# Kernel tuning notes

Measured on AMD Instinct MI355X. Metric: run time of the kernel, lower is better.

Reference implementation:

```python
import jax, jax.numpy as jnp
import numpy as np

T, B, IN, H1, HB = 512, 256, 64, 128, 32  # seq, batch, input, LSTM width, bottleneck


def _lstm(x, w_ih, w_hh, b_ih, b_hh):
    """Single-layer unidirectional LSTM, time-major x: [T,B,in] -> [T,B,H].
    PyTorch gate order: i, f, g, o. Zero initial state."""
    H = w_hh.shape[1]
    # hoist input projection out of the scan: [T,B,4H]
    xg = jnp.einsum('tbi,gi->tbg', x, w_ih) + b_ih + b_hh

    def step(carry, xt):
        h, c = carry
        g = xt + h @ w_hh.T
        i, f, gg, o = jnp.split(g, 4, axis=-1)
        c = jax.nn.sigmoid(f) * c + jax.nn.sigmoid(i) * jnp.tanh(gg)
        h = jax.nn.sigmoid(o) * jnp.tanh(c)
        return (h, c), h

    h0 = jnp.zeros((x.shape[1], H), x.dtype)
    (_, _), hs = jax.lax.scan(step, (h0, h0), xg)
    return hs


def setup_inputs() -> dict:
    key = jax.random.key(0)
    ks = jax.random.split(key, 17)
    s = 0.05

    def p(k, shape):
        return jax.random.normal(k, shape, dtype=jnp.float32) * s

    return {
        'X': jax.random.normal(ks[0], (T, B, IN), dtype=jnp.float32),
        # en1: IN -> H1
        'w1_ih': p(ks[1], (4 * H1, IN)), 'w1_hh': p(ks[2], (4 * H1, H1)),
        'b1_ih': p(ks[3], (4 * H1,)), 'b1_hh': p(ks[4], (4 * H1,)),
        # en2: H1 -> HB
        'w2_ih': p(ks[5], (4 * HB, H1)), 'w2_hh': p(ks[6], (4 * HB, HB)),
        'b2_ih': p(ks[7], (4 * HB,)), 'b2_hh': p(ks[8], (4 * HB,)),
        # de1: HB -> H1
        'w3_ih': p(ks[9], (4 * H1, HB)), 'w3_hh': p(ks[10], (4 * H1, H1)),
        'b3_ih': p(ks[11], (4 * H1,)), 'b3_hh': p(ks[12], (4 * H1,)),
        # de2: H1 -> IN
        'w4_ih': p(ks[13], (4 * IN, H1)), 'w4_hh': p(ks[14], (4 * IN, IN)),
        'b4_ih': p(ks[15], (4 * IN,)), 'b4_hh': p(ks[16], (4 * IN,)),
    }


def reference(X, w1_ih, w1_hh, b1_ih, b1_hh, w2_ih, w2_hh, b2_ih, b2_hh,
              w3_ih, w3_hh, b3_ih, b3_hh, w4_ih, w4_hh, b4_ih, b4_hh):
    h = _lstm(X, w1_ih, w1_hh, b1_ih, b1_hh)      # [T,B,128]
    h = _lstm(h, w2_ih, w2_hh, b2_ih, b2_hh)      # [T,B,32]
    h = jnp.tanh(h)                               # bottleneck tanh
    h = _lstm(h, w3_ih, w3_hh, b3_ih, b3_hh)      # [T,B,128]
    out = _lstm(h, w4_ih, w4_hh, b4_ih, b4_hh)    # [T,B,64]
    return out
```

## Files before the change

kernel.cpp:

```cpp
#include <hip/hip_runtime.h>

#define T_STEPS 512
#define BATCH   256

typedef _Float16 f16;
typedef unsigned long long u64;
typedef __attribute__((ext_vector_type(8))) _Float16 f16x8;
typedef __attribute__((ext_vector_type(4))) _Float16 f16x4;
typedef __attribute__((ext_vector_type(4))) float    f32x4;

__device__ __forceinline__ float rcp_f(float x) { return __builtin_amdgcn_rcpf(x); }
__device__ __forceinline__ float sigmoid_f(float x) { return rcp_f(1.0f + __expf(-x)); }
__device__ __forceinline__ float tanh_f(float x) {
    return 1.0f - 2.0f * rcp_f(__expf(2.0f * x) + 1.0f);
}

__device__ __forceinline__ void barrier_lgkm() {
    asm volatile("s_waitcnt lgkmcnt(0)\n\ts_barrier" ::: "memory");
}
__device__ __forceinline__ void barrier_drain() {
    asm volatile("s_waitcnt vmcnt(0) lgkmcnt(0)\n\ts_barrier" ::: "memory");
}

__device__ __forceinline__ int  flag_load(const int* p) {
    return __hip_atomic_load(p, __ATOMIC_RELAXED, __HIP_MEMORY_SCOPE_AGENT);
}
__device__ __forceinline__ void flag_store(int* p, int v) {
    __hip_atomic_store(p, v, __ATOMIC_RELAXED, __HIP_MEMORY_SCOPE_AGENT);
}
__device__ __forceinline__ u64  panel_load(const u64* p) {
    return __hip_atomic_load(p, __ATOMIC_RELAXED, __HIP_MEMORY_SCOPE_AGENT);
}
__device__ __forceinline__ void panel_store(u64* p, u64 v) {
    __hip_atomic_store(p, v, __ATOMIC_RELAXED, __HIP_MEMORY_SCOPE_AGENT);
}

__device__ __forceinline__ u64 tanh4_f16(u64 v) {
    f16x4 h = __builtin_bit_cast(f16x4, v);
    f16x4 r;
#pragma unroll
    for (int i = 0; i < 4; ++i) r[i] = (f16)tanh_f((float)h[i]);
    return __builtin_bit_cast(u64, r);
}

template <int IN_DIM, int H, bool IN_F32, bool OUT_PANEL, bool IN_TANH>
__device__ __forceinline__ void lstm_layer_dev(
    char* sm,
    const void* __restrict__ xv,
    const int* in_flag,
    int* out_flag,
    const float* __restrict__ w_ih, const float* __restrict__ w_hh,
    const float* __restrict__ b_ih, const float* __restrict__ b_hh,
    void* __restrict__ outv,
    int group, int ltid)
{
    constexpr int KTX = IN_DIM / 32, KTH = H / 32, KT = KTX + KTH;
    constexpr int XP = IN_DIM + 8, HP = H + 8, NT = 4 * H;

    f16 (*xs)[16][XP] = (f16(*)[16][XP])sm;
    f16 (*hs)[16][HP] = (f16(*)[16][HP])(sm + 2 * 16 * XP * 2);

    const int wave = ltid >> 6, lane = ltid & 63;
    const int col = lane & 15, q = lane >> 4;
    const int bblk = group * 16;
    const int u = wave * 16 + col;

    f16x8 bw[4][KT];
#pragma unroll
    for (int g = 0; g < 4; ++g) {
        const int row = g * H + u;
#pragma unroll
        for (int kt = 0; kt < KTX; ++kt) {
            const float* p = w_ih + (size_t)row * IN_DIM + kt * 32 + q * 8;
            f16x8 v;
#pragma unroll
            for (int j = 0; j < 8; ++j) v[j] = (f16)p[j];
            bw[g][kt] = v;
        }
#pragma unroll
        for (int kt = 0; kt < KTH; ++kt) {
            const float* p = w_hh + (size_t)row * H + kt * 32 + q * 8;
            f16x8 v;
#pragma unroll
            for (int j = 0; j < 8; ++j) v[j] = (f16)p[j];
            bw[g][KTX + kt] = v;
        }
    }
    float bias[4];
#pragma unroll
    for (int g = 0; g < 4; ++g) bias[g] = b_ih[g * H + u] + b_hh[g * H + u];
    float cst[4] = {0.f, 0.f, 0.f, 0.f};

    constexpr int EPR = IN_DIM / 4;
    constexpr int NCH = 16 * EPR;
    constexpr int CPT = (NCH + NT - 1) / NT;
    constexpr long XADVB = (long)BATCH * IN_DIM * (IN_F32 ? 4 : 2);
    bool sv[CPT]; const char* sgp[CPT]; f16* slp[CPT];
    constexpr int LDSD = 16 * XP;
#pragma unroll
    for (int k = 0; k < CPT; ++k) {
        const int cc = ltid + k * NT;
        sv[k] = (cc < NCH);
        const int r_ = (cc < NCH ? cc : 0) / EPR;
        const int o_ = (cc < NCH ? cc : 0) % EPR;
        sgp[k] = (const char*)xv + ((size_t)(bblk + r_) * IN_DIM + o_ * 4) * (IN_F32 ? 4 : 2);
        slp[k] = &xs[0][r_][o_ * 4];
    }

    constexpr int OEPR = H / 4;
    u64* opg = nullptr;
    f16* olds = nullptr;
    float* outp_f32 = nullptr;
    if constexpr (OUT_PANEL) {
        const int orow = ltid / OEPR, ooff = ltid % OEPR;
        opg  = (u64*)((f16*)outv + (size_t)(bblk + orow) * H) + ooff;
        olds = &hs[0][orow][ooff * 4];
    } else {
        outp_f32 = (float*)outv + ((size_t)bblk + 4 * q) * H + u;
    }
    constexpr int HLDSD = 16 * HP;

    for (int i = ltid; i < 16 * HP; i += NT) hs[0][i / HP][i % HP] = (f16)0.f;
    int seen = 0;
    if constexpr (!IN_F32) {
        do { seen = flag_load(in_flag); } while (seen < 1);
    }
#pragma unroll
    for (int k = 0; k < CPT; ++k) {
        if (sv[k]) {
            if constexpr (IN_F32) {
                const f32x4 v = *reinterpret_cast<const f32x4*>(sgp[k]);
                f16x4 h4;
                h4[0] = (f16)v[0]; h4[1] = (f16)v[1]; h4[2] = (f16)v[2]; h4[3] = (f16)v[3];
                *reinterpret_cast<f16x4*>(slp[k]) = h4;
            } else {
                u64 v = panel_load((const u64*)sgp[k]);
                if constexpr (IN_TANH) v = tanh4_f16(v);
                *reinterpret_cast<u64*>(slp[k]) = v;
            }
            sgp[k] += XADVB;
        }
    }
    barrier_drain();

    float hold[4] = {0.f, 0.f, 0.f, 0.f};
    int pb = 0;
    for (int t = 0; t < T_STEPS; ++t) {
        if constexpr (OUT_PANEL) {
            if ((t & 3) == 0 && t >= 4 && ltid == 0) flag_store(out_flag, t - 1);
        }

        f32x4 xr32[CPT]; u64 xr16[CPT];
        const bool pf = (t + 1 < T_STEPS);
        if (pf) {
            if constexpr (!IN_F32) {
                if (seen < t + 2) {
                    do { seen = flag_load(in_flag); } while (seen < t + 2);
                }
            }
#pragma unroll
            for (int k = 0; k < CPT; ++k) {
                if (sv[k]) {
                    if constexpr (IN_F32)
                        xr32[k] = *reinterpret_cast<const f32x4*>(sgp[k]);
                    else
                        xr16[k] = panel_load((const u64*)sgp[k]);
                    sgp[k] += XADVB;
                }
            }
        }

        if (t >= 1) {
            if constexpr (OUT_PANEL) {
                const u64 v = *reinterpret_cast<const u64*>(olds + pb * HLDSD);
                panel_store(opg, v);
                opg += (size_t)BATCH * H / 4;
            } else {
#pragma unroll
                for (int r = 0; r < 4; ++r) outp_f32[r * H] = hold[r];
                outp_f32 += (size_t)BATCH * H;
            }
        }

        f16x8 a[KT];
#pragma unroll
        for (int kt = 0; kt < KTX; ++kt)
            a[kt] = *reinterpret_cast<const f16x8*>(&xs[pb][col][kt * 32 + q * 8]);
#pragma unroll
        for (int kt = 0; kt < KTH; ++kt)
            a[KTX + kt] = *reinterpret_cast<const f16x8*>(&hs[pb][col][kt * 32 + q * 8]);

        f32x4 acc[4];
#pragma unroll
        for (int g = 0; g < 4; ++g)
            acc[g] = (f32x4){bias[g], bias[g], bias[g], bias[g]};
#pragma unroll
        for (int kt = 0; kt < KT; ++kt)
#pragma unroll
            for (int g = 0; g < 4; ++g)
                acc[g] = __builtin_amdgcn_mfma_f32_16x16x32_f16(a[kt], bw[g][kt], acc[g], 0, 0, 0);

#pragma unroll
        for (int r = 0; r < 4; ++r) {
            const float gi = acc[0][r];
            const float gf = acc[1][r];
            const float gg = acc[2][r];
            const float go = acc[3][r];
            cst[r] = sigmoid_f(gf) * cst[r] + sigmoid_f(gi) * tanh_f(gg);
            const float h = sigmoid_f(go) * tanh_f(cst[r]);
            hs[pb ^ 1][4 * q + r][u] = (f16)h;
            if constexpr (!OUT_PANEL) hold[r] = h;
        }

        if (pf) {
#pragma unroll
            for (int k = 0; k < CPT; ++k) {
                if (sv[k]) {
                    f16* dst = slp[k] + (pb ^ 1) * LDSD;
                    if constexpr (IN_F32) {
                        f16x4 h4;
                        h4[0] = (f16)xr32[k][0]; h4[1] = (f16)xr32[k][1];
                        h4[2] = (f16)xr32[k][2]; h4[3] = (f16)xr32[k][3];
                        *reinterpret_cast<f16x4*>(dst) = h4;
                    } else {
                        u64 v = xr16[k];
                        if constexpr (IN_TANH) v = tanh4_f16(v);
                        *reinterpret_cast<u64*>(dst) = v;
                    }
                }
            }
        }

        if constexpr (!IN_F32) {
            if (seen < t + 8) seen = flag_load(in_flag);
        }

        if ((t & 3) == 3) barrier_drain(); else barrier_lgkm();
        pb ^= 1;
    }

    if constexpr (OUT_PANEL) {
        const u64 v = *reinterpret_cast<const u64*>(olds + pb * HLDSD);
        panel_store(opg, v);
    } else {
#pragma unroll
        for (int r = 0; r < 4; ++r) outp_f32[r * H] = hold[r];
    }
    barrier_drain();
    if constexpr (OUT_PANEL) {
        if (ltid == 0) flag_store(out_flag, T_STEPS + 4);
    }
}

__global__ __launch_bounds__(512, 1)
void lstm_fused(const float* __restrict__ X,
                const float* __restrict__ w1_ih, const float* __restrict__ w1_hh,
                const float* __restrict__ b1_ih, const float* __restrict__ b1_hh,
                const float* __restrict__ w2_ih, const float* __restrict__ w2_hh,
                const float* __restrict__ b2_ih, const float* __restrict__ b2_hh,
                const float* __restrict__ w3_ih, const float* __restrict__ w3_hh,
                const float* __restrict__ b3_ih, const float* __restrict__ b3_hh,
                const float* __restrict__ w4_ih, const float* __restrict__ w4_hh,
                const float* __restrict__ b4_ih, const float* __restrict__ b4_hh,
                f16* __restrict__ h1, f16* __restrict__ h2, f16* __restrict__ h3,
                int* __restrict__ flags, float* __restrict__ out)
{
    __shared__ __attribute__((aligned(16))) char smem[45056];
    const int b = blockIdx.x, tid = threadIdx.x;

    if (b < 16) {
        lstm_layer_dev<64, 128, true, true, false>(
            smem, X, nullptr, flags + 0 * 16 + b,
            w1_ih, w1_hh, b1_ih, b1_hh, h1, b, tid);
    } else if (b < 20) {
        const int gl = tid >> 7;
        const int g  = (b - 16) * 4 + gl;
        lstm_layer_dev<128, 32, false, true, false>(
            smem + gl * 11264, h1, flags + 0 * 16 + g, flags + 1 * 16 + g,
            w2_ih, w2_hh, b2_ih, b2_hh, h2, g, tid & 127);
    } else if (b < 36) {
        const int g = b - 20;
        lstm_layer_dev<32, 128, false, true, true>(
            smem, h2, flags + 1 * 16 + g, flags + 2 * 16 + g,
            w3_ih, w3_hh, b3_ih, b3_hh, h3, g, tid);
    } else {
        const int gl = tid >> 8;
        const int g  = (b - 36) * 2 + gl;
        lstm_layer_dev<128, 64, false, false, false>(
            smem + gl * 13312, h3, flags + 2 * 16 + g, nullptr,
            w4_ih, w4_hh, b4_ih, b4_hh, out, g, tid & 255);
    }
}

extern "C" void kernel_launch(void* const* d_in, const int* in_sizes, int n_in,
                              void* d_out, int out_size, void* d_ws, size_t ws_size,
                              hipStream_t stream) {
    const float* X     = (const float*)d_in[0];
    const float* w1_ih = (const float*)d_in[1];
    const float* w1_hh = (const float*)d_in[2];
    const float* b1_ih = (const float*)d_in[3];
    const float* b1_hh = (const float*)d_in[4];
    const float* w2_ih = (const float*)d_in[5];
    const float* w2_hh = (const float*)d_in[6];
    const float* b2_ih = (const float*)d_in[7];
    const float* b2_hh = (const float*)d_in[8];
    const float* w3_ih = (const float*)d_in[9];
    const float* w3_hh = (const float*)d_in[10];
    const float* b3_ih = (const float*)d_in[11];
    const float* b3_hh = (const float*)d_in[12];
    const float* w4_ih = (const float*)d_in[13];
    const float* w4_hh = (const float*)d_in[14];
    const float* b4_ih = (const float*)d_in[15];
    const float* b4_hh = (const float*)d_in[16];

    float* out = (float*)d_out;

    int* flags = (int*)d_ws;
    f16* h1 = (f16*)((char*)d_ws + 256);
    f16* h2 = h1 + (size_t)T_STEPS * BATCH * 128;
    f16* h3 = h2 + (size_t)T_STEPS * BATCH * 32;

    lstm_fused<<<44, 512, 0, stream>>>(X,
        w1_ih, w1_hh, b1_ih, b1_hh, w2_ih, w2_hh, b2_ih, b2_hh,
        w3_ih, w3_hh, b3_ih, b3_hh, w4_ih, w4_hh, b4_ih, b4_hh,
        h1, h2, h3, flags, out);
}
```

Measured before the change: 760.9 us.

## Fold log2e into weights, use exp2 activations, move bottleneck tanh to producer, unroll by four

Gate weights and biases are pre-scaled by log2(e), or 2·log2(e) for the g gate, so the activations can use raw exp2 and rcp with fewer multiplies. The bottleneck tanh moves from the consumer layer (de1) to the publishing side of en2, and panel loads widen to 16-byte chunks per thread. The time loop is unrolled by four with compile-time buffer parity, drain and publish decisions, which removes per-step branching. The exp2-domain cell state carries scaled values, so it needs checking against the rounding introduced by the scaled f16 weights.

```diff
diff --git a/kernel.cpp b/kernel.cpp
--- a/kernel.cpp
+++ b/kernel.cpp
@@ -9,41 +9,43 @@
 typedef __attribute__((ext_vector_type(4))) _Float16 f16x4;
 typedef __attribute__((ext_vector_type(4))) float    f32x4;
 
-__device__ __forceinline__ float rcp_f(float x) { return __builtin_amdgcn_rcpf(x); }
-__device__ __forceinline__ float sigmoid_f(float x) { return rcp_f(1.0f + __expf(-x)); }
-__device__ __forceinline__ float tanh_f(float x) {
-    return 1.0f - 2.0f * rcp_f(__expf(2.0f * x) + 1.0f);
-}
-
-__device__ __forceinline__ void barrier_lgkm() {
-    asm volatile("s_waitcnt lgkmcnt(0)\n\ts_barrier" ::: "memory");
-}
-__device__ __forceinline__ void barrier_drain() {
-    asm volatile("s_waitcnt vmcnt(0) lgkmcnt(0)\n\ts_barrier" ::: "memory");
-}
-
-__device__ __forceinline__ int  flag_load(const int* p) {
-    return __hip_atomic_load(p, __ATOMIC_RELAXED, __HIP_MEMORY_SCOPE_AGENT);
-}
-__device__ __forceinline__ void flag_store(int* p, int v) {
-    __hip_atomic_store(p, v, __ATOMIC_RELAXED, __HIP_MEMORY_SCOPE_AGENT);
-}
-__device__ __forceinline__ u64  panel_load(const u64* p) {
-    return __hip_atomic_load(p, __ATOMIC_RELAXED, __HIP_MEMORY_SCOPE_AGENT);
-}
-__device__ __forceinline__ void panel_store(u64* p, u64 v) {
-    __hip_atomic_store(p, v, __ATOMIC_RELAXED, __HIP_MEMORY_SCOPE_AGENT);
-}
-
+#define L2E 1.44269504088896340736f
+
+__device__ __forceinline__ float rcp_f(float x)  { return __builtin_amdgcn_rcpf(x); }
+__device__ __forceinline__ float exp2_f(float x) { return __builtin_amdgcn_exp2f(x); }
+
+__device__ __forceinline__ float tanh_n(float x) {
+    return fmaf(-2.0f, rcp_f(1.0f + exp2_f(2.0f * L2E * x)), 1.0f);
+}
 __device__ __forceinline__ u64 tanh4_f16(u64 v) {
     f16x4 h = __builtin_bit_cast(f16x4, v);
     f16x4 r;
 #pragma unroll
-    for (int i = 0; i < 4; ++i) r[i] = (f16)tanh_f((float)h[i]);
+    for (int i = 0; i < 4; ++i) r[i] = (f16)tanh_n((float)h[i]);
     return __builtin_bit_cast(u64, r);
 }
 
-template <int IN_DIM, int H, bool IN_F32, bool OUT_PANEL, bool IN_TANH>
+__device__ __forceinline__ void barrier_lgkm() {
+    asm volatile("s_waitcnt lgkmcnt(0)\n\ts_barrier" ::: "memory");
+}
+__device__ __forceinline__ void barrier_drain() {
+    asm volatile("s_waitcnt vmcnt(0) lgkmcnt(0)\n\ts_barrier" ::: "memory");
+}
+
+__device__ __forceinline__ int  flag_load(const int* p) {
+    return __hip_atomic_load(p, __ATOMIC_RELAXED, __HIP_MEMORY_SCOPE_AGENT);
+}
+__device__ __forceinline__ void flag_store(int* p, int v) {
+    __hip_atomic_store(p, v, __ATOMIC_RELAXED, __HIP_MEMORY_SCOPE_AGENT);
+}
+__device__ __forceinline__ u64  panel_load(const u64* p) {
+    return __hip_atomic_load(p, __ATOMIC_RELAXED, __HIP_MEMORY_SCOPE_AGENT);
+}
+__device__ __forceinline__ void panel_store(u64* p, u64 v) {
+    __hip_atomic_store(p, v, __ATOMIC_RELAXED, __HIP_MEMORY_SCOPE_AGENT);
+}
+
+template <int IN_DIM, int H, bool IN_F32, bool OUT_PANEL, bool OUT_TANH>
 __device__ __forceinline__ void lstm_layer_dev(
     char* sm,
     const void* __restrict__ xv,
@@ -68,13 +70,14 @@
     f16x8 bw[4][KT];
 #pragma unroll
     for (int g = 0; g < 4; ++g) {
+        const float sc = (g == 2) ? 2.0f * L2E : L2E;
         const int row = g * H + u;
 #pragma unroll
         for (int kt = 0; kt < KTX; ++kt) {
             const float* p = w_ih + (size_t)row * IN_DIM + kt * 32 + q * 8;
             f16x8 v;
 #pragma unroll
-            for (int j = 0; j < 8; ++j) v[j] = (f16)p[j];
+            for (int j = 0; j < 8; ++j) v[j] = (f16)(p[j] * sc);
             bw[g][kt] = v;
         }
 #pragma unroll
@@ -82,16 +85,18 @@
             const float* p = w_hh + (size_t)row * H + kt * 32 + q * 8;
             f16x8 v;
 #pragma unroll
-            for (int j = 0; j < 8; ++j) v[j] = (f16)p[j];
+            for (int j = 0; j < 8; ++j) v[j] = (f16)(p[j] * sc);
             bw[g][KTX + kt] = v;
         }
     }
     float bias[4];
 #pragma unroll
-    for (int g = 0; g < 4; ++g) bias[g] = b_ih[g * H + u] + b_hh[g * H + u];
+    for (int g = 0; g < 4; ++g)
+        bias[g] = (b_ih[g * H + u] + b_hh[g * H + u]) * ((g == 2) ? 2.0f * L2E : L2E);
     float cst[4] = {0.f, 0.f, 0.f, 0.f};
 
-    constexpr int EPR = IN_DIM / 4;
+    constexpr int ELD = IN_F32 ? 4 : 8;
+    constexpr int EPR = IN_DIM / ELD;
     constexpr int NCH = 16 * EPR;
     constexpr int CPT = (NCH + NT - 1) / NT;
     constexpr long XADVB = (long)BATCH * IN_DIM * (IN_F32 ? 4 : 2);
@@ -103,8 +108,8 @@
         sv[k] = (cc < NCH);
         const int r_ = (cc < NCH ? cc : 0) / EPR;
         const int o_ = (cc < NCH ? cc : 0) % EPR;
-        sgp[k] = (const char*)xv + ((size_t)(bblk + r_) * IN_DIM + o_ * 4) * (IN_F32 ? 4 : 2);
-        slp[k] = &xs[0][r_][o_ * 4];
+        sgp[k] = (const char*)xv + ((size_t)(bblk + r_) * IN_DIM + o_ * ELD) * (IN_F32 ? 4 : 2);
+        slp[k] = &xs[0][r_][o_ * ELD];
     }
 
     constexpr int OEPR = H / 4;
@@ -134,9 +139,10 @@
                 h4[0] = (f16)v[0]; h4[1] = (f16)v[1]; h4[2] = (f16)v[2]; h4[3] = (f16)v[3];
                 *reinterpret_cast<f16x4*>(slp[k]) = h4;
             } else {
-                u64 v = panel_load((const u64*)sgp[k]);
-                if constexpr (IN_TANH) v = tanh4_f16(v);
-                *reinterpret_cast<u64*>(slp[k]) = v;
+                u64 a = panel_load((const u64*)sgp[k]);
+                u64 b = panel_load((const u64*)sgp[k] + 1);
+                u64 pk[2] = {a, b};
+                *reinterpret_cast<f16x8*>(slp[k]) = *reinterpret_cast<const f16x8*>(pk);
             }
             sgp[k] += XADVB;
         }
@@ -144,13 +150,13 @@
     barrier_drain();
 
     float hold[4] = {0.f, 0.f, 0.f, 0.f};
-    int pb = 0;
-    for (int t = 0; t < T_STEPS; ++t) {
+
+    auto step = [&](int t, int pbv, bool dodrain, bool dopub) {
         if constexpr (OUT_PANEL) {
-            if ((t & 3) == 0 && t >= 4 && ltid == 0) flag_store(out_flag, t - 1);
-        }
-
-        f32x4 xr32[CPT]; u64 xr16[CPT];
+            if (dopub && t >= 4 && ltid == 0) flag_store(out_flag, t - 1);
+        }
+
+        f32x4 xr32[CPT]; u64 xr16[CPT][2];
         const bool pf = (t + 1 < T_STEPS);
         if (pf) {
             if constexpr (!IN_F32) {
@@ -161,10 +167,12 @@
 #pragma unroll
             for (int k = 0; k < CPT; ++k) {
                 if (sv[k]) {
-                    if constexpr (IN_F32)
+                    if constexpr (IN_F32) {
                         xr32[k] = *reinterpret_cast<const f32x4*>(sgp[k]);
-                    else
-                        xr16[k] = panel_load((const u64*)sgp[k]);
+                    } else {
+                        xr16[k][0] = panel_load((const u64*)sgp[k]);
+                        xr16[k][1] = panel_load((const u64*)sgp[k] + 1);
+                    }
                     sgp[k] += XADVB;
                 }
             }
@@ -172,7 +180,8 @@
 
         if (t >= 1) {
             if constexpr (OUT_PANEL) {
-                const u64 v = *reinterpret_cast<const u64*>(olds + pb * HLDSD);
+                u64 v = *reinterpret_cast<const u64*>(olds + pbv * HLDSD);
+                if constexpr (OUT_TANH) v = tanh4_f16(v);
                 panel_store(opg, v);
                 opg += (size_t)BATCH * H / 4;
             } else {
@@ -185,10 +194,10 @@
         f16x8 a[KT];
 #pragma unroll
         for (int kt = 0; kt < KTX; ++kt)
-            a[kt] = *reinterpret_cast<const f16x8*>(&xs[pb][col][kt * 32 + q * 8]);
+            a[kt] = *reinterpret_cast<const f16x8*>(&xs[pbv][col][kt * 32 + q * 8]);
 #pragma unroll
         for (int kt = 0; kt < KTH; ++kt)
-            a[KTX + kt] = *reinterpret_cast<const f16x8*>(&hs[pb][col][kt * 32 + q * 8]);
+            a[KTX + kt] = *reinterpret_cast<const f16x8*>(&hs[pbv][col][kt * 32 + q * 8]);
 
         f32x4 acc[4];
 #pragma unroll
@@ -202,13 +211,20 @@
 
 #pragma unroll
         for (int r = 0; r < 4; ++r) {
-            const float gi = acc[0][r];
-            const float gf = acc[1][r];
-            const float gg = acc[2][r];
-            const float go = acc[3][r];
-            cst[r] = sigmoid_f(gf) * cst[r] + sigmoid_f(gi) * tanh_f(gg);
-            const float h = sigmoid_f(go) * tanh_f(cst[r]);
-            hs[pb ^ 1][4 * q + r][u] = (f16)h;
+            const float yi = acc[0][r];
+            const float yf = acc[1][r];
+            const float yg = acc[2][r];
+            const float yo = acc[3][r];
+            const float si = rcp_f(1.0f + exp2_f(-yi));
+            const float sf = rcp_f(1.0f + exp2_f(-yf));
+            const float dg = rcp_f(1.0f + exp2_f(yg));
+            const float tgp = fmaf(dg, -4.0f * L2E, 2.0f * L2E);
+            cst[r] = fmaf(sf, cst[r], si * tgp);
+            const float dc = rcp_f(1.0f + exp2_f(cst[r]));
+            const float th = fmaf(-2.0f, dc, 1.0f);
+            const float so = rcp_f(1.0f + exp2_f(-yo));
+            const float h = so * th;
+            hs[pbv ^ 1][4 * q + r][u] = (f16)h;
             if constexpr (!OUT_PANEL) hold[r] = h;
         }
 
@@ -216,31 +232,37 @@
 #pragma unroll
             for (int k = 0; k < CPT; ++k) {
                 if (sv[k]) {
-                    f16* dst = slp[k] + (pb ^ 1) * LDSD;
+                    f16* dst = slp[k] + (pbv ^ 1) * LDSD;
                     if constexpr (IN_F32) {
                         f16x4 h4;
                         h4[0] = (f16)xr32[k][0]; h4[1] = (f16)xr32[k][1];
                         h4[2] = (f16)xr32[k][2]; h4[3] = (f16)xr32[k][3];
                         *reinterpret_cast<f16x4*>(dst) = h4;
                     } else {
-                        u64 v = xr16[k];
-                        if constexpr (IN_TANH) v = tanh4_f16(v);
-                        *reinterpret_cast<u64*>(dst) = v;
+                        *reinterpret_cast<f16x8*>(dst) =
+                            *reinterpret_cast<const f16x8*>(xr16[k]);
                     }
                 }
             }
         }
 
         if constexpr (!IN_F32) {
-            if (seen < t + 8) seen = flag_load(in_flag);
-        }
-
-        if ((t & 3) == 3) barrier_drain(); else barrier_lgkm();
-        pb ^= 1;
+            if (dopub && seen < t + 9) seen = flag_load(in_flag);
+        }
+
+        if (dodrain) barrier_drain(); else barrier_lgkm();
+    };
+
+    for (int tb = 0; tb < T_STEPS; tb += 4) {
+        step(tb + 0, 0, false, true);
+        step(tb + 1, 1, false, false);
+        step(tb + 2, 0, false, false);
+        step(tb + 3, 1, true,  false);
     }
 
     if constexpr (OUT_PANEL) {
-        const u64 v = *reinterpret_cast<const u64*>(olds + pb * HLDSD);
+        u64 v = *reinterpret_cast<const u64*>(olds);
+        if constexpr (OUT_TANH) v = tanh4_f16(v);
         panel_store(opg, v);
     } else {
 #pragma unroll
@@ -275,12 +297,12 @@
     } else if (b < 20) {
         const int gl = tid >> 7;
         const int g  = (b - 16) * 4 + gl;
-        lstm_layer_dev<128, 32, false, true, false>(
+        lstm_layer_dev<128, 32, false, true, true>(
             smem + gl * 11264, h1, flags + 0 * 16 + g, flags + 1 * 16 + g,
             w2_ih, w2_hh, b2_ih, b2_hh, h2, g, tid & 127);
     } else if (b < 36) {
         const int g = b - 20;
-        lstm_layer_dev<32, 128, false, true, true>(
+        lstm_layer_dev<32, 128, false, true, false>(
             smem, h2, flags + 1 * 16 + g, flags + 2 * 16 + g,
             w3_ih, w3_hh, b3_ih, b3_hh, h3, g, tid);
     } else {
```

Result: faster. 649.4 us (-14.7%).
